# Kernel optimization log

Hardware: AMD Instinct MI355X
Metric: run time of the kernel (lower is better)

The kernel has to match this reference:

```python
import jax, jax.numpy as jnp
import numpy as np
from math import sqrt


def setup_inputs() -> dict:
    key = jax.random.key(0)
    ks = jax.random.split(key, 10)
    N, C = 192, 96  # C = N // 2
    n, h, w = 8, 64, 64
    s = lambda fan_in: 1.0 / np.sqrt(fan_in)
    return {
        "x": jax.random.normal(ks[0], (n, N, h, w), dtype=jnp.float32),
        "pe": jax.random.normal(ks[1], (N, 120, 120), dtype=jnp.float32) * 0.02,
        "wq": jax.random.normal(ks[2], (C, N), dtype=jnp.float32) * s(N),
        "bq": jax.random.normal(ks[3], (C,), dtype=jnp.float32) * 0.01,
        "wk": jax.random.normal(ks[4], (C, N), dtype=jnp.float32) * s(N),
        "bk": jax.random.normal(ks[5], (C,), dtype=jnp.float32) * 0.01,
        "wv": jax.random.normal(ks[6], (C, N), dtype=jnp.float32) * s(N),
        "bv": jax.random.normal(ks[7], (C,), dtype=jnp.float32) * 0.01,
        "wz": jax.random.normal(ks[8], (N, C), dtype=jnp.float32) * s(C),
        "bz": jax.random.normal(ks[9], (N,), dtype=jnp.float32) * 0.01,
    }


def _conv1x1(x, w, b):
    # x: [n, cin, h, w]; w: [cout, cin]; b: [cout]
    return jnp.einsum("oc,nchw->nohw", w, x) + b[None, :, None, None]


def reference(x, pe, wq, bq, wk, bk, wv, bv, wz, bz):
    n, c_in, h, w = x.shape
    hw = h * w
    # 2D positional encoding, sliced to the actual spatial size
    x = x + pe[None, :, :h, :w]
    c = wq.shape[0]  # N // 2
    q = _conv1x1(x, wq, bq).reshape(n, c, hw)   # [n, c, hw]
    k = _conv1x1(x, wk, bk).reshape(n, c, hw)   # [n, c, hw]
    v = _conv1x1(x, wv, bv).reshape(n, c, hw)   # [n, c, hw]
    scale = sqrt(hw)
    # logits[n, i, j] = sum_c q[n,c,i] * k[n,c,j]
    logits = jnp.einsum("nci,ncj->nij", q, k) / scale  # [n, hw, hw]
    weights = jax.nn.softmax(logits, axis=-1)
    # z[n, c, i] = sum_j weights[n,i,j] * v[n,c,j]
    z = jnp.einsum("nij,ncj->nci", weights, v).reshape(n, c, h, w)
    z = _conv1x1(z, wz, bz)  # [n, N, h, w]
    return x + z
```

## Files before the change

### kernel.cpp

```cpp
#include <hip/hip_runtime.h>
#include <hip/hip_bf16.h>

#define HW 4096
#define CIN 192
#define CMID 96

typedef __attribute__((ext_vector_type(8))) short bf16x8;
typedef __attribute__((ext_vector_type(4))) float f32x4;
typedef __attribute__((ext_vector_type(16))) float f32x16;
typedef __attribute__((ext_vector_type(4))) unsigned int u32x4;

static __device__ __forceinline__ unsigned short f2bf(float f) {
    union { float f; unsigned int u; } v;
    v.f = f;
    unsigned int r = v.u + 0x7fffu + ((v.u >> 16) & 1u);
    return (unsigned short)(r >> 16);
}
static __device__ __forceinline__ float b2f(unsigned short h) {
    union { unsigned int u; float f; } v;
    v.u = ((unsigned int)h) << 16;
    return v.f;
}

static __device__ __forceinline__ void gload16(const void* g, void* l) {
    __builtin_amdgcn_global_load_lds(
        (const __attribute__((address_space(1))) unsigned int*)g,
        (__attribute__((address_space(3))) unsigned int*)l, 16, 0, 0);
}

#define SCQ (0.015625f * 1.44269504089f)

__global__ __launch_bounds__(256) void convw_kernel(
    const float* __restrict__ wq, const float* __restrict__ wk,
    const float* __restrict__ wv, const float* __restrict__ wz,
    unsigned short* __restrict__ wqkvb, unsigned short* __restrict__ wzb)
{
    int idx = blockIdx.x * 256 + threadIdx.x;
    if (idx < 3 * CMID * CIN) {
        int m = idx / (CMID * CIN), r = idx % (CMID * CIN);
        const float* w = (m == 0) ? wq : ((m == 1) ? wk : wv);
        wqkvb[idx] = f2bf(w[r]);
    } else if (idx < 3 * CMID * CIN + CIN * CMID) {
        int r = idx - 3 * CMID * CIN;
        wzb[r] = f2bf(wz[r]);
    }
}

__global__ __launch_bounds__(256) void qkv_kernel(
    const float* __restrict__ x, const float* __restrict__ pe,
    const unsigned short* __restrict__ wqkvb,
    const float* __restrict__ bq, const float* __restrict__ bk,
    const float* __restrict__ bv,
    unsigned short* __restrict__ Q, unsigned short* __restrict__ K,
    unsigned short* __restrict__ V)
{
    const int n = blockIdx.y, i0 = blockIdx.x * 64, t = threadIdx.x;
    __shared__ unsigned short xt[64 * 200];

    for (int idx = t; idx < CIN * 64; idx += 256) {
        int c = idx >> 6, il = idx & 63;
        float v = x[((size_t)n * CIN + c) * HW + i0 + il]
                + pe[c * 14400 + blockIdx.x * 120 + il];
        xt[il * 200 + c] = f2bf(v);
    }
    __syncthreads();

    const int w = t >> 6, lane = t & 63, l15 = lane & 15, lg = lane >> 4;
    const int p0 = w * 16;

    bf16x8 af[6];
    #pragma unroll
    for (int f = 0; f < 6; ++f)
        af[f] = *(const bf16x8*)(xt + (p0 + l15) * 200 + f * 32 + lg * 8);

    #pragma unroll
    for (int ct = 0; ct < 18; ++ct) {
        const int m = ct / 6, c6 = ct % 6;
        f32x4 acc = (f32x4){0.f, 0.f, 0.f, 0.f};
        const unsigned short* wrow = wqkvb + (ct * 16 + l15) * CIN + lg * 8;
        #pragma unroll
        for (int f = 0; f < 6; ++f) {
            bf16x8 wf = *(const bf16x8*)(wrow + f * 32);
            if (m < 2)
                acc = __builtin_amdgcn_mfma_f32_16x16x32_bf16(wf, af[f], acc, 0, 0, 0);
            else
                acc = __builtin_amdgcn_mfma_f32_16x16x32_bf16(af[f], wf, acc, 0, 0, 0);
        }
        if (m < 2) {
            f32x4 bv4 = *(const f32x4*)(((m == 0) ? bq : bk) + c6 * 16 + lg * 4);
            ushort4 pk4;
            if (m == 0) {
                pk4.x = f2bf((acc[0] + bv4[0]) * SCQ);
                pk4.y = f2bf((acc[1] + bv4[1]) * SCQ);
                pk4.z = f2bf((acc[2] + bv4[2]) * SCQ);
                pk4.w = f2bf((acc[3] + bv4[3]) * SCQ);
            } else {
                pk4.x = f2bf(acc[0] + bv4[0]);
                pk4.y = f2bf(acc[1] + bv4[1]);
                pk4.z = f2bf(acc[2] + bv4[2]);
                pk4.w = f2bf(acc[3] + bv4[3]);
            }
            unsigned short* dst = ((m == 0) ? Q : K) + (size_t)n * HW * CMID;
            *(ushort4*)(dst + (size_t)(i0 + p0 + l15) * CMID + c6 * 16 + lg * 4) = pk4;
        } else {
            const float bias = bv[c6 * 16 + l15];
            ushort4 pk4;
            pk4.x = f2bf(acc[0] + bias); pk4.y = f2bf(acc[1] + bias);
            pk4.z = f2bf(acc[2] + bias); pk4.w = f2bf(acc[3] + bias);
            *(ushort4*)(V + (size_t)n * CMID * HW + (size_t)(c6 * 16 + l15) * HW
                          + i0 + p0 + lg * 4) = pk4;
        }
    }
}

__global__ __launch_bounds__(256, 2) void attn_kernel(
    const unsigned short* __restrict__ Q, const unsigned short* __restrict__ K,
    const unsigned short* __restrict__ V,
    unsigned short* __restrict__ zp, float* __restrict__ lp)
{
    const int bid = blockIdx.x;
    const int xcd = bid & 7, kk_ = bid >> 3;
    const int g = xcd + 8 * (kk_ >> 5);
    const int bx = kk_ & 31;
    const int n = g >> 1, jh = g & 1;

    const int t = threadIdx.x, w = t >> 6, lane = t & 63;
    const int l31 = lane & 31, hi = lane >> 5;
    const int r7 = l31 & 7;
    const int ib = bx * 128 + w * 32;

    __shared__ unsigned short Ks[2][64 * 128];
    __shared__ unsigned short Vs[2][96 * 64];

    const unsigned short* Qb = Q + (size_t)n * HW * CMID;
    const unsigned short* Kb = K + (size_t)n * HW * CMID;
    const unsigned short* Vb = V + (size_t)n * CMID * HW;

    bf16x8 qf[6];
    #pragma unroll
    for (int kc = 0; kc < 6; ++kc)
        qf[kc] = *(const bf16x8*)(Qb + (size_t)(ib + l31) * CMID + kc * 16 + hi * 8);

    int ksoff[4], vsoff[3];
    #pragma unroll
    for (int s = 0; s < 4; ++s) {
        int row = 4 * (w * 4 + s) + (lane >> 4);
        ksoff[s] = row * CMID + (((lane & 15) ^ (row & 7)) * 8);
    }
    #pragma unroll
    for (int s = 0; s < 3; ++s) {
        int c = 8 * (w * 3 + s) + (lane >> 3);
        vsoff[s] = c * HW + (((lane & 7) ^ (c & 7)) * 8);
    }

#define STAGE(J0, BUF) do {                                                        \
    _Pragma("unroll") for (int s = 0; s < 4; ++s)                                  \
        gload16(Kb + (size_t)(J0) * CMID + ksoff[s], &Ks[BUF][(w * 4 + s) * 512]); \
    _Pragma("unroll") for (int s = 0; s < 3; ++s)                                  \
        gload16(Vb + (size_t)(J0) + vsoff[s], &Vs[BUF][(w * 3 + s) * 512]);        \
} while (0)

    const int j00 = jh * 2048;
    STAGE(j00, 0);

    f32x16 O[3], Lon;
    #pragma unroll
    for (int e = 0; e < 16; ++e) { O[0][e] = 0.f; O[1][e] = 0.f; O[2][e] = 0.f; Lon[e] = 0.f; }

    bf16x8 onef;
    #pragma unroll
    for (int e = 0; e < 8; ++e) onef[e] = (short)0x3F80;

    __syncthreads();

    for (int tt = 0; tt < 32; ++tt) {
        if (tt < 31) STAGE(j00 + (tt + 1) * 64, (tt + 1) & 1);

        const unsigned short* Kc = Ks[tt & 1];
        const unsigned short* Vc = Vs[tt & 1];

        f32x16 sacc[2];
        __builtin_amdgcn_s_setprio(1);
        #pragma unroll
        for (int s = 0; s < 2; ++s) {
            f32x16 a;
            #pragma unroll
            for (int e = 0; e < 16; ++e) a[e] = 0.f;
            const int row = s * 32 + l31;
            #pragma unroll
            for (int kc = 0; kc < 6; ++kc) {
                bf16x8 kf = *(const bf16x8*)(Kc + row * 128 + ((((kc * 2 + hi) ^ r7)) << 3));
                a = __builtin_amdgcn_mfma_f32_32x32x16_bf16(kf, qf[kc], a, 0, 0, 0);
            }
            sacc[s] = a;
        }
        __builtin_amdgcn_s_setprio(0);

        unsigned pkk[2][4][2];
        #pragma unroll
        for (int s = 0; s < 2; ++s)
            #pragma unroll
            for (int q = 0; q < 4; ++q)
                #pragma unroll
                for (int rp = 0; rp < 2; ++rp) {
                    float lo = exp2f(sacc[s][q * 4 + 2 * rp]);
                    float hh = exp2f(sacc[s][q * 4 + 2 * rp + 1]);
                    unsigned d;
                    asm("v_cvt_pk_bf16_f32 %0, %1, %2" : "=v"(d) : "v"(lo), "v"(hh));
                    pkk[s][q][rp] = d;
                }

        u32x4 pfu[4];
        #pragma unroll
        for (int s = 0; s < 2; ++s)
            #pragma unroll
            for (int p = 0; p < 2; ++p)
                #pragma unroll
                for (int rp = 0; rp < 2; ++rp) {
                    unsigned A = pkk[s][2 * p][rp], B = pkk[s][2 * p + 1][rp];
                    unsigned Ax = (unsigned)__shfl_xor((int)A, 32, 64);
                    unsigned Bx = (unsigned)__shfl_xor((int)B, 32, 64);
                    pfu[s * 2 + p][rp]     = hi ? Bx : A;
                    pfu[s * 2 + p][2 + rp] = hi ? B  : Ax;
                }

        __builtin_amdgcn_s_setprio(1);
        #pragma unroll
        for (int jc = 0; jc < 4; ++jc) {
            bf16x8 pfv = __builtin_bit_cast(bf16x8, pfu[jc]);
            #pragma unroll
            for (int cc = 0; cc < 3; ++cc) {
                const int row = cc * 32 + l31;
                bf16x8 vf = *(const bf16x8*)(Vc + row * 64 + ((((jc * 2 + hi) ^ r7)) << 3));
                O[cc] = __builtin_amdgcn_mfma_f32_32x32x16_bf16(pfv, vf, O[cc], 0, 0, 0);
            }
            Lon = __builtin_amdgcn_mfma_f32_32x32x16_bf16(pfv, onef, Lon, 0, 0, 0);
        }
        __builtin_amdgcn_s_setprio(0);

        __syncthreads();
    }
#undef STAGE

    unsigned short* zb = zp + ((size_t)jh * 8 + n) * HW * CMID;
    #pragma unroll
    for (int cc = 0; cc < 3; ++cc)
        #pragma unroll
        for (int r = 0; r < 16; ++r) {
            int i = (r & 3) + 8 * (r >> 2) + 4 * hi;
            zb[(size_t)(ib + i) * CMID + cc * 32 + l31] = f2bf(O[cc][r]);
        }
    if (l31 == 0) {
        float* lb = lp + ((size_t)jh * 8 + n) * HW;
        #pragma unroll
        for (int r = 0; r < 16; ++r) {
            int i = (r & 3) + 8 * (r >> 2) + 4 * hi;
            lb[ib + i] = Lon[r];
        }
    }
}

__global__ __launch_bounds__(256) void zproj_kernel(
    const unsigned short* __restrict__ zp, const float* __restrict__ lp,
    const unsigned short* __restrict__ wzb, const float* __restrict__ bz,
    const float* __restrict__ x, const float* __restrict__ pe,
    float* __restrict__ out)
{
    const int n = blockIdx.y, i0 = blockIdx.x * 64, t = threadIdx.x;
    __shared__ unsigned short zt[64 * 104];
    __shared__ float ll[64];

    const unsigned short* zp0 = zp;
    const unsigned short* zp1 = zp + (size_t)8 * HW * CMID;
    const float* lp0 = lp;
    const float* lp1 = lp + (size_t)8 * HW;

    if (t < 64)
        ll[t] = 1.f / (lp0[(size_t)n * HW + i0 + t] + lp1[(size_t)n * HW + i0 + t]);
    __syncthreads();

    for (int idx = t; idx < 64 * 24; idx += 256) {
        int i = idx / 24, c4 = (idx % 24) * 4;
        size_t gidx = ((size_t)n * HW + i0 + i) * CMID + c4;
        ushort4 a = *(const ushort4*)(zp0 + gidx);
        ushort4 b = *(const ushort4*)(zp1 + gidx);
        float li = ll[i];
        zt[i * 104 + c4 + 0] = f2bf((b2f(a.x) + b2f(b.x)) * li);
        zt[i * 104 + c4 + 1] = f2bf((b2f(a.y) + b2f(b.y)) * li);
        zt[i * 104 + c4 + 2] = f2bf((b2f(a.z) + b2f(b.z)) * li);
        zt[i * 104 + c4 + 3] = f2bf((b2f(a.w) + b2f(b.w)) * li);
    }
    __syncthreads();

    const int w = t >> 6, lane = t & 63, l15 = lane & 15, lg = lane >> 4;
    const int p0 = w * 16;

    bf16x8 af[3];
    #pragma unroll
    for (int f = 0; f < 3; ++f)
        af[f] = *(const bf16x8*)(zt + (p0 + l15) * 104 + f * 32 + lg * 8);

    #pragma unroll
    for (int ct = 0; ct < 12; ++ct) {
        f32x4 acc = (f32x4){0.f, 0.f, 0.f, 0.f};
        const unsigned short* wrow = wzb + (ct * 16 + l15) * CMID + lg * 8;
        #pragma unroll
        for (int f = 0; f < 3; ++f) {
            bf16x8 wf = *(const bf16x8*)(wrow + f * 32);
            acc = __builtin_amdgcn_mfma_f32_16x16x32_bf16(af[f], wf, acc, 0, 0, 0);
        }
        const int co = ct * 16 + l15;
        const int ibase = i0 + p0 + lg * 4;
        size_t xa = ((size_t)n * CIN + co) * HW + ibase;
        f32x4 xv = *(const f32x4*)(x + xa);
        f32x4 pv = *(const f32x4*)(pe + co * 14400 + blockIdx.x * 120 + p0 + lg * 4);
        const float bias = bz[co];
        f32x4 o;
        #pragma unroll
        for (int r = 0; r < 4; ++r) o[r] = xv[r] + pv[r] + acc[r] + bias;
        *(f32x4*)(out + xa) = o;
    }
}

extern "C" void kernel_launch(void* const* d_in, const int* in_sizes, int n_in,
                              void* d_out, int out_size, void* d_ws, size_t ws_size,
                              hipStream_t stream) {
    const float* x  = (const float*)d_in[0];
    const float* pe = (const float*)d_in[1];
    const float* wq = (const float*)d_in[2];
    const float* bq = (const float*)d_in[3];
    const float* wk = (const float*)d_in[4];
    const float* bk = (const float*)d_in[5];
    const float* wv = (const float*)d_in[6];
    const float* bv = (const float*)d_in[7];
    const float* wz = (const float*)d_in[8];
    const float* bz = (const float*)d_in[9];
    float* out = (float*)d_out;

    char* ws = (char*)d_ws;
    unsigned short* wqkvb = (unsigned short*)(ws);
    unsigned short* wzb   = (unsigned short*)(ws + 131072);
    unsigned short* Qb    = (unsigned short*)(ws + 196608);
    unsigned short* Kb    = (unsigned short*)(ws + 6488064);
    unsigned short* Vb    = (unsigned short*)(ws + 12779520);
    unsigned short* zpb   = (unsigned short*)(ws + 19070976);
    float*          lpb   = (float*)(ws + 31653888);

    convw_kernel<<<288, 256, 0, stream>>>(wq, wk, wv, wz, wqkvb, wzb);
    qkv_kernel<<<dim3(64, 8), 256, 0, stream>>>(x, pe, wqkvb, bq, bk, bv,
                                                Qb, Kb, Vb);
    attn_kernel<<<512, 256, 0, stream>>>(Qb, Kb, Vb, zpb, lpb);
    zproj_kernel<<<dim3(64, 8), 256, 0, stream>>>(zpb, lpb, wzb, bz, x, pe, out);
}
```

Measured before the change: 129.9 us.

## Split attention keys into four slices with smaller tiles and scalar row sums

Splits the key dimension four ways instead of two, launching 1024 blocks with 32-key K tiles and V tiles reloaded every other step. Occupancy rises to 4 blocks per CU. The MFMA-with-ones row-sum accumulator is replaced by scalar accumulation of exp values, which frees registers. The z projection now reduces four partial outputs, which adds workspace traffic. The block-to-XCD mapping is also simplified to n = bid & 7.

```diff
diff --git a/kernel.cpp b/kernel.cpp
--- a/kernel.cpp
+++ b/kernel.cpp
@@ -113,23 +113,21 @@
     }
 }
 
-__global__ __launch_bounds__(256, 2) void attn_kernel(
+__global__ __launch_bounds__(256, 4) void attn_kernel(
     const unsigned short* __restrict__ Q, const unsigned short* __restrict__ K,
     const unsigned short* __restrict__ V,
     unsigned short* __restrict__ zp, float* __restrict__ lp)
 {
     const int bid = blockIdx.x;
-    const int xcd = bid & 7, kk_ = bid >> 3;
-    const int g = xcd + 8 * (kk_ >> 5);
-    const int bx = kk_ & 31;
-    const int n = g >> 1, jh = g & 1;
+    const int n  = bid & 7;
+    const int jh = bid >> 8;
+    const int bx = (bid >> 3) & 31;
 
     const int t = threadIdx.x, w = t >> 6, lane = t & 63;
     const int l31 = lane & 31, hi = lane >> 5;
-    const int r7 = l31 & 7;
     const int ib = bx * 128 + w * 32;
 
-    __shared__ unsigned short Ks[2][64 * 128];
+    __shared__ unsigned short Ks[2][32 * 128];
     __shared__ unsigned short Vs[2][96 * 64];
 
     const unsigned short* Qb = Q + (size_t)n * HW * CMID;
@@ -141,10 +139,10 @@
     for (int kc = 0; kc < 6; ++kc)
         qf[kc] = *(const bf16x8*)(Qb + (size_t)(ib + l31) * CMID + kc * 16 + hi * 8);
 
-    int ksoff[4], vsoff[3];
-    #pragma unroll
-    for (int s = 0; s < 4; ++s) {
-        int row = 4 * (w * 4 + s) + (lane >> 4);
+    int ksoff[2], vsoff[3];
+    #pragma unroll
+    for (int s = 0; s < 2; ++s) {
+        int row = 4 * (w * 2 + s) + (lane >> 4);
         ksoff[s] = row * CMID + (((lane & 15) ^ (row & 7)) * 8);
     }
     #pragma unroll
@@ -153,94 +151,89 @@
         vsoff[s] = c * HW + (((lane & 7) ^ (c & 7)) * 8);
     }
 
-#define STAGE(J0, BUF) do {                                                        \
-    _Pragma("unroll") for (int s = 0; s < 4; ++s)                                  \
-        gload16(Kb + (size_t)(J0) * CMID + ksoff[s], &Ks[BUF][(w * 4 + s) * 512]); \
+#define STAGE_K(J0, BUF) do {                                                      \
+    _Pragma("unroll") for (int s = 0; s < 2; ++s)                                  \
+        gload16(Kb + (size_t)(J0) * CMID + ksoff[s], &Ks[BUF][(w * 2 + s) * 512]); \
+} while (0)
+#define STAGE_V(J0, BUF) do {                                                      \
     _Pragma("unroll") for (int s = 0; s < 3; ++s)                                  \
         gload16(Vb + (size_t)(J0) + vsoff[s], &Vs[BUF][(w * 3 + s) * 512]);        \
 } while (0)
 
-    const int j00 = jh * 2048;
-    STAGE(j00, 0);
-
-    f32x16 O[3], Lon;
-    #pragma unroll
-    for (int e = 0; e < 16; ++e) { O[0][e] = 0.f; O[1][e] = 0.f; O[2][e] = 0.f; Lon[e] = 0.f; }
-
-    bf16x8 onef;
-    #pragma unroll
-    for (int e = 0; e < 8; ++e) onef[e] = (short)0x3F80;
+    const int j00 = jh * 1024;
+    STAGE_K(j00, 0);
+    STAGE_V(j00, 0);
+
+    f32x16 O[3];
+    #pragma unroll
+    for (int e = 0; e < 16; ++e) { O[0][e] = 0.f; O[1][e] = 0.f; O[2][e] = 0.f; }
+    float lsum = 0.f;
 
     __syncthreads();
 
     for (int tt = 0; tt < 32; ++tt) {
-        if (tt < 31) STAGE(j00 + (tt + 1) * 64, (tt + 1) & 1);
+        if (tt < 31) STAGE_K(j00 + (tt + 1) * 32, (tt + 1) & 1);
+        if ((tt & 1) == 0 && tt < 30)
+            STAGE_V(j00 + ((tt >> 1) + 1) * 64, ((tt >> 1) + 1) & 1);
 
         const unsigned short* Kc = Ks[tt & 1];
-        const unsigned short* Vc = Vs[tt & 1];
-
-        f32x16 sacc[2];
+        const unsigned short* Vc = Vs[(tt >> 1) & 1];
+        const int vhalf = tt & 1;
+
+        f32x16 sacc;
+        #pragma unroll
+        for (int e = 0; e < 16; ++e) sacc[e] = 0.f;
         __builtin_amdgcn_s_setprio(1);
         #pragma unroll
-        for (int s = 0; s < 2; ++s) {
-            f32x16 a;
+        for (int kc = 0; kc < 6; ++kc) {
+            bf16x8 kf = *(const bf16x8*)(Kc + l31 * 128
+                                           + ((((kc * 2 + hi) ^ (l31 & 7))) << 3));
+            sacc = __builtin_amdgcn_mfma_f32_32x32x16_bf16(kf, qf[kc], sacc, 0, 0, 0);
+        }
+        __builtin_amdgcn_s_setprio(0);
+
+        unsigned pkk[4][2];
+        #pragma unroll
+        for (int q = 0; q < 4; ++q)
             #pragma unroll
-            for (int e = 0; e < 16; ++e) a[e] = 0.f;
-            const int row = s * 32 + l31;
+            for (int rp = 0; rp < 2; ++rp) {
+                float lo = exp2f(sacc[q * 4 + 2 * rp]);
+                float hh = exp2f(sacc[q * 4 + 2 * rp + 1]);
+                lsum += lo + hh;
+                unsigned d;
+                asm("v_cvt_pk_bf16_f32 %0, %1, %2" : "=v"(d) : "v"(lo), "v"(hh));
+                pkk[q][rp] = d;
+            }
+
+        u32x4 pfu[2];
+        #pragma unroll
+        for (int p = 0; p < 2; ++p)
             #pragma unroll
-            for (int kc = 0; kc < 6; ++kc) {
-                bf16x8 kf = *(const bf16x8*)(Kc + row * 128 + ((((kc * 2 + hi) ^ r7)) << 3));
-                a = __builtin_amdgcn_mfma_f32_32x32x16_bf16(kf, qf[kc], a, 0, 0, 0);
+            for (int rp = 0; rp < 2; ++rp) {
+                unsigned A = pkk[2 * p][rp], B = pkk[2 * p + 1][rp];
+                unsigned Ax = (unsigned)__shfl_xor((int)A, 32, 64);
+                unsigned Bx = (unsigned)__shfl_xor((int)B, 32, 64);
+                pfu[p][rp]     = hi ? Bx : A;
+                pfu[p][2 + rp] = hi ? B  : Ax;
             }
-            sacc[s] = a;
-        }
-        __builtin_amdgcn_s_setprio(0);
-
-        unsigned pkk[2][4][2];
-        #pragma unroll
-        for (int s = 0; s < 2; ++s)
-            #pragma unroll
-            for (int q = 0; q < 4; ++q)
-                #pragma unroll
-                for (int rp = 0; rp < 2; ++rp) {
-                    float lo = exp2f(sacc[s][q * 4 + 2 * rp]);
-                    float hh = exp2f(sacc[s][q * 4 + 2 * rp + 1]);
-                    unsigned d;
-                    asm("v_cvt_pk_bf16_f32 %0, %1, %2" : "=v"(d) : "v"(lo), "v"(hh));
-                    pkk[s][q][rp] = d;
-                }
-
-        u32x4 pfu[4];
-        #pragma unroll
-        for (int s = 0; s < 2; ++s)
-            #pragma unroll
-            for (int p = 0; p < 2; ++p)
-                #pragma unroll
-                for (int rp = 0; rp < 2; ++rp) {
-                    unsigned A = pkk[s][2 * p][rp], B = pkk[s][2 * p + 1][rp];
-                    unsigned Ax = (unsigned)__shfl_xor((int)A, 32, 64);
-                    unsigned Bx = (unsigned)__shfl_xor((int)B, 32, 64);
-                    pfu[s * 2 + p][rp]     = hi ? Bx : A;
-                    pfu[s * 2 + p][2 + rp] = hi ? B  : Ax;
-                }
 
         __builtin_amdgcn_s_setprio(1);
         #pragma unroll
-        for (int jc = 0; jc < 4; ++jc) {
+        for (int jc = 0; jc < 2; ++jc) {
             bf16x8 pfv = __builtin_bit_cast(bf16x8, pfu[jc]);
             #pragma unroll
             for (int cc = 0; cc < 3; ++cc) {
-                const int row = cc * 32 + l31;
-                bf16x8 vf = *(const bf16x8*)(Vc + row * 64 + ((((jc * 2 + hi) ^ r7)) << 3));
+                bf16x8 vf = *(const bf16x8*)(Vc + (cc * 32 + l31) * 64
+                    + ((((vhalf * 4 + jc * 2 + hi) ^ (l31 & 7))) << 3));
                 O[cc] = __builtin_amdgcn_mfma_f32_32x32x16_bf16(pfv, vf, O[cc], 0, 0, 0);
             }
-            Lon = __builtin_amdgcn_mfma_f32_32x32x16_bf16(pfv, onef, Lon, 0, 0, 0);
         }
         __builtin_amdgcn_s_setprio(0);
 
         __syncthreads();
     }
-#undef STAGE
+#undef STAGE_K
+#undef STAGE_V
 
     unsigned short* zb = zp + ((size_t)jh * 8 + n) * HW * CMID;
     #pragma unroll
@@ -250,13 +243,11 @@
             int i = (r & 3) + 8 * (r >> 2) + 4 * hi;
             zb[(size_t)(ib + i) * CMID + cc * 32 + l31] = f2bf(O[cc][r]);
         }
-    if (l31 == 0) {
+
+    lsum += __shfl_xor(lsum, 32, 64);
+    if (hi == 0) {
         float* lb = lp + ((size_t)jh * 8 + n) * HW;
-        #pragma unroll
-        for (int r = 0; r < 16; ++r) {
-            int i = (r & 3) + 8 * (r >> 2) + 4 * hi;
-            lb[ib + i] = Lon[r];
-        }
+        lb[ib + l31] = lsum;
     }
 }
 
@@ -270,25 +261,29 @@
     __shared__ unsigned short zt[64 * 104];
     __shared__ float ll[64];
 
-    const unsigned short* zp0 = zp;
-    const unsigned short* zp1 = zp + (size_t)8 * HW * CMID;
-    const float* lp0 = lp;
-    const float* lp1 = lp + (size_t)8 * HW;
-
-    if (t < 64)
-        ll[t] = 1.f / (lp0[(size_t)n * HW + i0 + t] + lp1[(size_t)n * HW + i0 + t]);
+    if (t < 64) {
+        float s = 0.f;
+        #pragma unroll
+        for (int sl = 0; sl < 4; ++sl)
+            s += lp[(size_t)sl * 8 * HW + (size_t)n * HW + i0 + t];
+        ll[t] = 1.f / s;
+    }
     __syncthreads();
 
     for (int idx = t; idx < 64 * 24; idx += 256) {
         int i = idx / 24, c4 = (idx % 24) * 4;
         size_t gidx = ((size_t)n * HW + i0 + i) * CMID + c4;
-        ushort4 a = *(const ushort4*)(zp0 + gidx);
-        ushort4 b = *(const ushort4*)(zp1 + gidx);
+        float a0 = 0.f, a1 = 0.f, a2 = 0.f, a3 = 0.f;
+        #pragma unroll
+        for (int sl = 0; sl < 4; ++sl) {
+            ushort4 a = *(const ushort4*)(zp + (size_t)sl * 8 * HW * CMID + gidx);
+            a0 += b2f(a.x); a1 += b2f(a.y); a2 += b2f(a.z); a3 += b2f(a.w);
+        }
         float li = ll[i];
-        zt[i * 104 + c4 + 0] = f2bf((b2f(a.x) + b2f(b.x)) * li);
-        zt[i * 104 + c4 + 1] = f2bf((b2f(a.y) + b2f(b.y)) * li);
-        zt[i * 104 + c4 + 2] = f2bf((b2f(a.z) + b2f(b.z)) * li);
-        zt[i * 104 + c4 + 3] = f2bf((b2f(a.w) + b2f(b.w)) * li);
+        zt[i * 104 + c4 + 0] = f2bf(a0 * li);
+        zt[i * 104 + c4 + 1] = f2bf(a1 * li);
+        zt[i * 104 + c4 + 2] = f2bf(a2 * li);
+        zt[i * 104 + c4 + 3] = f2bf(a3 * li);
     }
     __syncthreads();
 
@@ -344,11 +339,11 @@
     unsigned short* Kb    = (unsigned short*)(ws + 6488064);
     unsigned short* Vb    = (unsigned short*)(ws + 12779520);
     unsigned short* zpb   = (unsigned short*)(ws + 19070976);
-    float*          lpb   = (float*)(ws + 31653888);
+    float*          lpb   = (float*)(ws + 44236800);
 
     convw_kernel<<<288, 256, 0, stream>>>(wq, wk, wv, wz, wqkvb, wzb);
     qkv_kernel<<<dim3(64, 8), 256, 0, stream>>>(x, pe, wqkvb, bq, bk, bv,
                                                 Qb, Kb, Vb);
-    attn_kernel<<<512, 256, 0, stream>>>(Qb, Kb, Vb, zpb, lpb);
+    attn_kernel<<<1024, 256, 0, stream>>>(Qb, Kb, Vb, zpb, lpb);
     zproj_kernel<<<dim3(64, 8), 256, 0, stream>>>(zpb, lpb, wzb, bz, x, pe, out);
 }
```

Result: no change. 130.2 us (+0.2%).
